# Kernel optimization log

Hardware: AMD Instinct MI355X
Metric: run time of the kernel (lower is better)

Reference implementation:

```python
import jax, jax.numpy as jnp
import numpy as np

N = 200000          # total instances
NUM_BAGS = 25000    # ragged bags, avg size 8
D = 690             # repre_size
R = 53              # rel_size


def setup_inputs() -> dict:
    key = jax.random.key(0)
    k1, k2, k3 = jax.random.split(key, 3)
    repre = jax.random.normal(k1, (N, D), dtype=jnp.float32)
    relation_mat = jax.random.normal(k2, (R, D), dtype=jnp.float32) * 0.001
    bias = jnp.zeros((R,), dtype=jnp.float32)
    labels = jax.random.randint(k3, (N,), 0, R, dtype=jnp.int64)
    # ragged contiguous scopes partitioning [0, N)
    rng = np.random.default_rng(0)
    cuts = np.sort(rng.choice(np.arange(1, N), size=NUM_BAGS - 1, replace=False))
    starts = np.concatenate([[0], cuts])
    ends = np.concatenate([cuts, [N]])
    scope = jnp.asarray(np.stack([starts, ends], axis=1), dtype=jnp.int64)
    return {"repre": repre, "relation_mat": relation_mat, "bias": bias,
            "scope": scope, "labels": labels}


def reference(repre, relation_mat, bias, scope, labels):
    # training / use_bag path of AttentionSelector.forward
    starts = scope[:, 0]
    # segment id for each instance (scopes are a contiguous partition)
    seg = jnp.searchsorted(starts, jnp.arange(N), side="right") - 1  # [N]
    rel_vecs = relation_mat[labels]                      # [N, D]
    rel_logits = jnp.sum(repre * rel_vecs, axis=-1)      # [N]
    # segment softmax (numerically stable)
    m = jax.ops.segment_max(rel_logits, seg, num_segments=NUM_BAGS)
    e = jnp.exp(rel_logits - m[seg])
    denom = jax.ops.segment_sum(e, seg, num_segments=NUM_BAGS)
    w = e / denom[seg]                                   # [N]
    att_repres = jax.ops.segment_sum(w[:, None] * repre, seg,
                                     num_segments=NUM_BAGS)  # [NUM_BAGS, D]
    logits = att_repres @ relation_mat.T + bias          # [NUM_BAGS, R]
    return logits
```

## Files before the change

### kernel.cpp

```cpp
#include <hip/hip_runtime.h>


#define NBAGS  25000
#define DDIM   690
#define D2     345
#define RREL   53
#define WAVES  8
#define BLOCK  512

__global__ __launch_bounds__(BLOCK, 4) void bag_attn_kernel(
    const float* __restrict__ repre,
    const float* __restrict__ rel,
    const float* __restrict__ bias,
    const int*   __restrict__ scope,
    const int*   __restrict__ labels,
    float*       __restrict__ out)
{
    __shared__ float s_att[WAVES * DDIM];

    const int tid  = threadIdx.x;
    const int lane = tid & 63;
    const int wave = tid >> 6;
    const int bag  = blockIdx.x * WAVES + wave;

    const int start = scope[2 * bag];
    const int end   = scope[2 * bag + 1];

    const float2* rel2 = (const float2*)rel;

    float2 acc[6];
    #pragma unroll
    for (int k = 0; k < 6; ++k) acc[k] = make_float2(0.f, 0.f);
    float m = -3.402823466e38f;
    float l = 0.f;

    for (int row = start; row < end; ++row) {
        const float2* rp = (const float2*)(repre + (size_t)row * DDIM);
        const float2* rl = rel2 + (size_t)labels[row] * D2;

        float2 v[6];
        float dot = 0.f;
        #pragma unroll
        for (int k = 0; k < 6; ++k) {
            const int f = lane + 64 * k;
            if (f < D2) {
                v[k] = rp[f];
                const float2 u = rl[f];
                dot = fmaf(v[k].x, u.x, fmaf(v[k].y, u.y, dot));
            } else {
                v[k] = make_float2(0.f, 0.f);
            }
        }
        #pragma unroll
        for (int o = 32; o; o >>= 1) dot += __shfl_xor(dot, o, 64);

        const float nm = fmaxf(m, dot);
        const float sc = __expf(m - nm);
        const float e  = __expf(dot - nm);
        l = fmaf(l, sc, e);
        #pragma unroll
        for (int k = 0; k < 6; ++k) {
            acc[k].x = fmaf(acc[k].x, sc, e * v[k].x);
            acc[k].y = fmaf(acc[k].y, sc, e * v[k].y);
        }
        m = nm;
    }

    const float inv = 1.f / l;
    float2* satt2 = (float2*)(s_att + wave * DDIM);
    #pragma unroll
    for (int k = 0; k < 6; ++k) {
        const int f = lane + 64 * k;
        if (f < D2) satt2[f] = make_float2(acc[k].x * inv, acc[k].y * inv);
    }
    __syncthreads();

    const int bag0 = blockIdx.x * WAVES;
    for (int r = wave; r < RREL; r += WAVES) {
        const float2* rl = rel2 + (size_t)r * D2;
        float2 u[6];
        #pragma unroll
        for (int k = 0; k < 6; ++k) {
            const int f = lane + 64 * k;
            u[k] = (f < D2) ? rl[f] : make_float2(0.f, 0.f);
        }
        const float b = bias[r];
        #pragma unroll
        for (int g = 0; g < WAVES; ++g) {
            const float2* a2 = (const float2*)(s_att + g * DDIM);
            float dot = 0.f;
            #pragma unroll
            for (int k = 0; k < 6; ++k) {
                const int f = lane + 64 * k;
                if (f < D2) {
                    const float2 a = a2[f];
                    dot = fmaf(u[k].x, a.x, fmaf(u[k].y, a.y, dot));
                }
            }
            #pragma unroll
            for (int o = 32; o; o >>= 1) dot += __shfl_xor(dot, o, 64);
            if (lane == 0) out[(size_t)(bag0 + g) * RREL + r] = dot + b;
        }
    }
}

extern "C" void kernel_launch(void* const* d_in, const int* in_sizes, int n_in,
                              void* d_out, int out_size, void* d_ws, size_t ws_size,
                              hipStream_t stream)
{
    const float* repre  = (const float*)d_in[0];
    const float* rel    = (const float*)d_in[1];
    const float* bias   = (const float*)d_in[2];
    const int*   scope  = (const int*)d_in[3];
    const int*   labels = (const int*)d_in[4];
    float*       out    = (float*)d_out;

    const int grid = NBAGS / WAVES;
    bag_attn_kernel<<<grid, BLOCK, 0, stream>>>(repre, rel, bias, scope, labels, out);
}
```

Measured before the change: 994.5 us.

## Dynamically schedule 16 bags per block and unroll rows by two

Each block now owns 16 bags, and its 8 waves pull bags from a shared atomic counter. This is meant to even out work across ragged bag sizes. The per-row loop handles two instances at once to expose more memory-level parallelism, and it drops the running-max rescaling of the online softmax. That last step means exp() is taken on raw logits, which can overflow for large logits. The final projection reuses each relation row against all 16 bag vectors with register accumulators, batching the shuffle reductions.

```diff
diff --git a/kernel.cpp b/kernel.cpp
--- a/kernel.cpp
+++ b/kernel.cpp
@@ -5,6 +5,7 @@
 #define DDIM   690
 #define D2     345
 #define RREL   53
+#define GB     16
 #define WAVES  8
 #define BLOCK  512
 
@@ -16,66 +17,110 @@
     const int*   __restrict__ labels,
     float*       __restrict__ out)
 {
-    __shared__ float s_att[WAVES * DDIM];
+    __shared__ float s_att[GB * DDIM];
+    __shared__ int   s_next;
 
     const int tid  = threadIdx.x;
     const int lane = tid & 63;
     const int wave = tid >> 6;
-    const int bag  = blockIdx.x * WAVES + wave;
+    const int bag0 = blockIdx.x * GB;
 
-    const int start = scope[2 * bag];
-    const int end   = scope[2 * bag + 1];
+    if (tid == 0) s_next = 0;
+    __syncthreads();
 
     const float2* rel2 = (const float2*)rel;
 
-    float2 acc[6];
-    #pragma unroll
-    for (int k = 0; k < 6; ++k) acc[k] = make_float2(0.f, 0.f);
-    float m = -3.402823466e38f;
-    float l = 0.f;
+    for (;;) {
+        int g;
+        if (lane == 0) g = atomicAdd(&s_next, 1);
+        g = __shfl(g, 0, 64);
+        if (g >= GB) break;
+        const int bag = bag0 + g;
+        if (bag >= NBAGS) break;
 
-    for (int row = start; row < end; ++row) {
-        const float2* rp = (const float2*)(repre + (size_t)row * DDIM);
-        const float2* rl = rel2 + (size_t)labels[row] * D2;
+        const int start = scope[2 * bag];
+        const int end   = scope[2 * bag + 1];
 
-        float2 v[6];
-        float dot = 0.f;
+        float2 acc[6];
+        #pragma unroll
+        for (int k = 0; k < 6; ++k) acc[k] = make_float2(0.f, 0.f);
+        float l = 0.f;
+
+        int row = start;
+        for (; row + 2 <= end; row += 2) {
+            const float2* rp0 = (const float2*)(repre + (size_t)row * DDIM);
+            const float2* rp1 = rp0 + D2;
+            const float2* rl0 = rel2 + (size_t)labels[row] * D2;
+            const float2* rl1 = rel2 + (size_t)labels[row + 1] * D2;
+
+            float2 v0[6], v1[6];
+            float d0 = 0.f, d1 = 0.f;
+            #pragma unroll
+            for (int k = 0; k < 6; ++k) {
+                const int f = lane + 64 * k;
+                if (f < D2) {
+                    v0[k] = rp0[f];
+                    v1[k] = rp1[f];
+                    const float2 u0 = rl0[f];
+                    const float2 u1 = rl1[f];
+                    d0 = fmaf(v0[k].x, u0.x, fmaf(v0[k].y, u0.y, d0));
+                    d1 = fmaf(v1[k].x, u1.x, fmaf(v1[k].y, u1.y, d1));
+                } else {
+                    v0[k] = make_float2(0.f, 0.f);
+                    v1[k] = make_float2(0.f, 0.f);
+                }
+            }
+            #pragma unroll
+            for (int o = 32; o; o >>= 1) {
+                d0 += __shfl_xor(d0, o, 64);
+                d1 += __shfl_xor(d1, o, 64);
+            }
+            const float e0 = __expf(d0);
+            const float e1 = __expf(d1);
+            l += e0 + e1;
+            #pragma unroll
+            for (int k = 0; k < 6; ++k) {
+                acc[k].x = fmaf(e0, v0[k].x, fmaf(e1, v1[k].x, acc[k].x));
+                acc[k].y = fmaf(e0, v0[k].y, fmaf(e1, v1[k].y, acc[k].y));
+            }
+        }
+        if (row < end) {
+            const float2* rp0 = (const float2*)(repre + (size_t)row * DDIM);
+            const float2* rl0 = rel2 + (size_t)labels[row] * D2;
+            float2 v0[6];
+            float d0 = 0.f;
+            #pragma unroll
+            for (int k = 0; k < 6; ++k) {
+                const int f = lane + 64 * k;
+                if (f < D2) {
+                    v0[k] = rp0[f];
+                    const float2 u0 = rl0[f];
+                    d0 = fmaf(v0[k].x, u0.x, fmaf(v0[k].y, u0.y, d0));
+                } else {
+                    v0[k] = make_float2(0.f, 0.f);
+                }
+            }
+            #pragma unroll
+            for (int o = 32; o; o >>= 1) d0 += __shfl_xor(d0, o, 64);
+            const float e0 = __expf(d0);
+            l += e0;
+            #pragma unroll
+            for (int k = 0; k < 6; ++k) {
+                acc[k].x = fmaf(e0, v0[k].x, acc[k].x);
+                acc[k].y = fmaf(e0, v0[k].y, acc[k].y);
+            }
+        }
+
+        const float inv = 1.f / l;
+        float2* sa = (float2*)(s_att + g * DDIM);
         #pragma unroll
         for (int k = 0; k < 6; ++k) {
             const int f = lane + 64 * k;
-            if (f < D2) {
-                v[k] = rp[f];
-                const float2 u = rl[f];
-                dot = fmaf(v[k].x, u.x, fmaf(v[k].y, u.y, dot));
-            } else {
-                v[k] = make_float2(0.f, 0.f);
-            }
+            if (f < D2) sa[f] = make_float2(acc[k].x * inv, acc[k].y * inv);
         }
-        #pragma unroll
-        for (int o = 32; o; o >>= 1) dot += __shfl_xor(dot, o, 64);
-
-        const float nm = fmaxf(m, dot);
-        const float sc = __expf(m - nm);
-        const float e  = __expf(dot - nm);
-        l = fmaf(l, sc, e);
-        #pragma unroll
-        for (int k = 0; k < 6; ++k) {
-            acc[k].x = fmaf(acc[k].x, sc, e * v[k].x);
-            acc[k].y = fmaf(acc[k].y, sc, e * v[k].y);
-        }
-        m = nm;
-    }
-
-    const float inv = 1.f / l;
-    float2* satt2 = (float2*)(s_att + wave * DDIM);
-    #pragma unroll
-    for (int k = 0; k < 6; ++k) {
-        const int f = lane + 64 * k;
-        if (f < D2) satt2[f] = make_float2(acc[k].x * inv, acc[k].y * inv);
     }
     __syncthreads();
 
-    const int bag0 = blockIdx.x * WAVES;
     for (int r = wave; r < RREL; r += WAVES) {
         const float2* rl = rel2 + (size_t)r * D2;
         float2 u[6];
@@ -84,22 +129,33 @@
             const int f = lane + 64 * k;
             u[k] = (f < D2) ? rl[f] : make_float2(0.f, 0.f);
         }
-        const float b = bias[r];
+        float acc[GB];
         #pragma unroll
-        for (int g = 0; g < WAVES; ++g) {
-            const float2* a2 = (const float2*)(s_att + g * DDIM);
-            float dot = 0.f;
-            #pragma unroll
-            for (int k = 0; k < 6; ++k) {
-                const int f = lane + 64 * k;
-                if (f < D2) {
-                    const float2 a = a2[f];
-                    dot = fmaf(u[k].x, a.x, fmaf(u[k].y, a.y, dot));
+        for (int g = 0; g < GB; ++g) acc[g] = 0.f;
+        #pragma unroll
+        for (int k = 0; k < 6; ++k) {
+            const int f = lane + 64 * k;
+            if (f < D2) {
+                const float2 uu = u[k];
+                #pragma unroll
+                for (int g = 0; g < GB; ++g) {
+                    const float2 a = ((const float2*)(s_att + g * DDIM))[f];
+                    acc[g] = fmaf(uu.x, a.x, fmaf(uu.y, a.y, acc[g]));
                 }
             }
+        }
+        #pragma unroll
+        for (int o = 32; o; o >>= 1) {
             #pragma unroll
-            for (int o = 32; o; o >>= 1) dot += __shfl_xor(dot, o, 64);
-            if (lane == 0) out[(size_t)(bag0 + g) * RREL + r] = dot + b;
+            for (int g = 0; g < GB; ++g) acc[g] += __shfl_xor(acc[g], o, 64);
+        }
+        if (lane == 0) {
+            const float b = bias[r];
+            #pragma unroll
+            for (int g = 0; g < GB; ++g) {
+                const int bag = bag0 + g;
+                if (bag < NBAGS) out[(size_t)bag * RREL + r] = acc[g] + b;
+            }
         }
     }
 }
@@ -115,6 +171,6 @@
     const int*   labels = (const int*)d_in[4];
     float*       out    = (float*)d_out;
 
-    const int grid = NBAGS / WAVES;
+    const int grid = (NBAGS + GB - 1) / GB;
     bag_attn_kernel<<<grid, BLOCK, 0, stream>>>(repre, rel, bias, scope, labels, out);
 }
```

Result: slower. 1.228 ms (+23.5%).
